# Performance work log

Hardware: AMD Instinct MI355X
Metric: run time of the kernel (lower is better)

The kernel has to match this reference:

```python
import jax, jax.numpy as jnp
import numpy as np

EPS = 1e-8
NUM_LAYERS = 6


def setup_inputs() -> dict:
    key = jax.random.key(0)
    ks = jax.random.split(key, 8)
    N, Cin, Cout, S, H, W = 4, 256, 256, 512, 64, 64
    fan_in = Cin  # kaiming for 1x1 conv, leaky_relu a=0 -> gain sqrt(2)
    return {
        "x": jax.random.normal(ks[0], (N, Cin, H, W), dtype=jnp.float32),
        "y": jax.random.normal(ks[1], (N, S), dtype=jnp.float32),
        "ch_conv_w": jax.random.normal(ks[2], (Cout, Cin), dtype=jnp.float32) / np.sqrt(fan_in),
        "ch_conv_b": jnp.zeros((Cout,), dtype=jnp.float32),
        "affine_w": jax.random.normal(ks[3], (NUM_LAYERS, Cout, S), dtype=jnp.float32) / np.sqrt(S),
        "affine_b": jnp.zeros((NUM_LAYERS, Cout), dtype=jnp.float32),
        "mod_w": jax.random.normal(ks[4], (NUM_LAYERS, Cout, Cout), dtype=jnp.float32) * np.sqrt(2.0 / Cout),
    }


def _forward(x, y, ch_conv_w, ch_conv_b, affine_w, affine_b, mod_w):
    # 1x1 channel conv (with bias)
    x = jnp.einsum("oi,bihw->bohw", ch_conv_w, x) + ch_conv_b[None, :, None, None]
    x = jnp.repeat(jnp.repeat(x, 2, axis=2), 2, axis=3)
    # channel repeat_interleave(2) -> [N, 2C, H, W]
    x = jnp.repeat(x, 2, axis=1)

    C = x.shape[1] // 2
    for i in range(NUM_LAYERS):
        x1, x2 = x[:, :C], x[:, C:]
        # SpatialShift2d with default directions pads [1,1,1,1] (replicate) then
        # crops the identical region for every split -> exact identity.
        y1 = x1 + x2
        # g-branch: Conv2dMod(k=1) with per-sample style modulation + exact GELU
        s = jnp.einsum("cs,bs->bc", affine_w[i], y) + affine_b[i]  # [B, C]
        wmod = mod_w[i][None] * (s[:, :, None] + 1.0)              # [B, O, I] (style scales OUTPUT channel)
        d = jax.lax.rsqrt(jnp.sum(wmod * wmod, axis=2, keepdims=True) + EPS)
        wmod = wmod * d
        h = jnp.einsum("boi,bihw->bohw", wmod, y1)
        y2 = x2 + jax.nn.gelu(h, approximate=False)
        x = jnp.concatenate([y1, y2], axis=1)

    x1, x2 = x[:, :C], x[:, C:]
    return (x1 + x2) * 0.5


def reference(x, y, ch_conv_w, ch_conv_b, affine_w, affine_b, mod_w):
    return _forward(x, y, ch_conv_w, ch_conv_b, affine_w, affine_b, mod_w)
```

## Files before the change

### kernel.cpp

```cpp
#include <hip/hip_runtime.h>
#include <math.h>

#define NB 4
#define CC 256
#define SS 512
#define NL 6
#define SLOT_HW 65536

typedef __attribute__((ext_vector_type(8))) short s16x8;
typedef __attribute__((ext_vector_type(4))) float f32x4;
typedef __attribute__((ext_vector_type(4))) unsigned short u16x4;
typedef __attribute__((ext_vector_type(8))) unsigned short u16x8;

__device__ __forceinline__ unsigned short f2bf(float f) {
    unsigned u = __builtin_bit_cast(unsigned, f);
    u += 0x7FFFu + ((u >> 16) & 1u);
    return (unsigned short)(u >> 16);
}
__device__ __forceinline__ float bf2f(unsigned short h) {
    unsigned u = ((unsigned)h) << 16;
    return __builtin_bit_cast(float, u);
}
__device__ __forceinline__ float gelu_fast(float x) {
    float u = x * (1.0f + 0.044715f * x * x);
    float e = __expf(-1.5957691216f * u);
    return x / (1.0f + e);
}


__global__ __launch_bounds__(256) void wmod_kernel(
    const float* __restrict__ y, const float* __restrict__ aw,
    const float* __restrict__ ab, const float* __restrict__ mw,
    unsigned short* __restrict__ wsBF)
{
    int w = threadIdx.x >> 6, lane = threadIdx.x & 63;
    int r = blockIdx.x*4 + w;
    int l = r >> 10;
    int b = (r >> 8) & 3;
    int o = r & 255;

    const float* awr = aw + (size_t)(l*CC + o)*SS;
    const float* yb  = y + (size_t)b*SS;
    float s = 0.f;
#pragma unroll
    for (int j = 0; j < 8; ++j) { int idx = lane + 64*j; s += awr[idx]*yb[idx]; }
#pragma unroll
    for (int off = 32; off; off >>= 1) s += __shfl_xor(s, off);
    float t = s + ab[l*CC + o] + 1.0f;

    const float* mwr = mw + (size_t)(l*CC + o)*CC;
    float wv[4]; float ss = 0.f;
#pragma unroll
    for (int u = 0; u < 4; ++u) { int j = lane + 64*u; wv[u] = mwr[j]*t; ss += wv[u]*wv[u]; }
#pragma unroll
    for (int off = 32; off; off >>= 1) ss += __shfl_xor(ss, off);
    float d = 1.0f / sqrtf(ss + 1e-8f);

    unsigned short* slot = wsBF + (size_t)(1 + l*NB + b)*SLOT_HW;
#pragma unroll
    for (int u = 0; u < 4; ++u) {
        int k = lane + 64*u;
        int f = (o >> 4)*8 + (k >> 5);
        int hw = f*512 + ((k >> 3) & 3)*128 + (o & 15)*8 + (k & 7);
        slot[hw] = f2bf(wv[u]*d);
    }
}

__global__ __launch_bounds__(256) void cwsplit_kernel(
    const float* __restrict__ cw, unsigned short* __restrict__ wsBF)
{
    int w = threadIdx.x >> 6, lane = threadIdx.x & 63;
    int m = blockIdx.x*4 + w;
#pragma unroll
    for (int u = 0; u < 4; ++u) {
        int k = lane + 64*u;
        int f = (m >> 4)*8 + (k >> 5);
        int hw = f*512 + ((k >> 3) & 3)*128 + (m & 15)*8 + (k & 7);
        wsBF[hw] = f2bf(cw[(size_t)m*CC + k]);
    }
}

#define BFRAG(buf, nt, kcl, hl) \
    (lds + (buf)*16384 + ((((nt)*2 + (kcl))*2 + (hl)))*1024)

__global__ __launch_bounds__(512, 2) void fused_kernel(
    const float* __restrict__ x, const float* __restrict__ cb,
    const unsigned short* __restrict__ wsBF, float* __restrict__ out)
{
    __shared__ __align__(16) unsigned char lds[50176];
    float* xS = (float*)(lds + 32768);
    float* S2 = (float*)lds;

    const int tid  = threadIdx.x;
    const int lane = tid & 63;
    const int wid  = tid >> 6;
    const int wm   = wid >> 1;
    const int wn   = wid & 1;
    const int l15  = lane & 15;
    const int q    = lane >> 4;

    const int bswz  = blockIdx.x & 7;
    const int b     = bswz >> 1;
    const int strip = ((blockIdx.x >> 3) << 1) | (bswz & 1);
    const int n0    = strip * 64;

    float y1[4][2][4], y2[4][2][4];
    f32x4 acc[4][2];

#pragma unroll
    for (int t = 0; t < 4; ++t)
#pragma unroll
        for (int s = 0; s < 2; ++s) acc[t][s] = 0;

    for (int kq = 0; kq < 4; ++kq) {
        int buf = kq & 1;
        {
            int r0 = tid >> 4, c4 = (tid & 15) * 4;
#pragma unroll
            for (int p = 0; p < 2; ++p) {
                int row = r0 + 32*p;
                float4 v = *(const float4*)&x[((size_t)(b*CC + kq*64 + row))*4096 + n0 + c4];
                *(float4*)&xS[row*68 + c4] = v;
            }
        }
        __syncthreads();
        {
            int n = tid & 63, k0 = (tid >> 6) * 8;
            float f[8];
#pragma unroll
            for (int i = 0; i < 8; ++i) f[i] = xS[(k0+i)*68 + n];
            u16x8 hv, lv;
#pragma unroll
            for (int i = 0; i < 8; ++i) {
                unsigned short h = f2bf(f[i]);
                hv[i] = h; lv[i] = f2bf(f[i] - bf2f(h));
            }
            int nt = n >> 4, n15 = n & 15, kcl = k0 >> 5, qq = (k0 >> 3) & 3;
            *(u16x8*)(BFRAG(buf,nt,kcl,0) + (16*qq + n15)*16) = hv;
            *(u16x8*)(BFRAG(buf,nt,kcl,1) + (16*qq + n15)*16) = lv;
        }
        s16x8 afr[2][4];
#pragma unroll
        for (int kcl = 0; kcl < 2; ++kcl)
#pragma unroll
        for (int t = 0; t < 4; ++t)
            afr[kcl][t] = *(const s16x8*)(wsBF + (size_t)((4*wm+t)*8 + kq*2+kcl)*512 + lane*8);
        __syncthreads();
#pragma unroll
        for (int kcl = 0; kcl < 2; ++kcl)
#pragma unroll
        for (int s = 0; s < 2; ++s) {
            int nt = 2*wn + s;
            s16x8 bh = *(const s16x8*)(BFRAG(buf,nt,kcl,0) + lane*16);
            s16x8 bl = *(const s16x8*)(BFRAG(buf,nt,kcl,1) + lane*16);
#pragma unroll
            for (int t = 0; t < 4; ++t) {
                acc[t][s] = __builtin_amdgcn_mfma_f32_16x16x32_bf16(afr[kcl][t], bh, acc[t][s], 0, 0, 0);
                acc[t][s] = __builtin_amdgcn_mfma_f32_16x16x32_bf16(afr[kcl][t], bl, acc[t][s], 0, 0, 0);
            }
        }
    }

#pragma unroll
    for (int pass = 0; pass < 2; ++pass) {
        __syncthreads();
        if ((wm >> 1) == pass) {
#pragma unroll
            for (int t = 0; t < 4; ++t)
#pragma unroll
            for (int s = 0; s < 2; ++s)
#pragma unroll
            for (int r = 0; r < 4; ++r) {
                int m  = 64*wm + 16*t + 4*q + r;
                int nl = 32*wn + 16*s + l15;
                S2[(m - 128*pass)*66 + nl] = acc[t][s][r] + cb[m];
            }
        }
        __syncthreads();
#pragma unroll
        for (int t = 0; t < 4; ++t)
#pragma unroll
        for (int s = 0; s < 2; ++s)
#pragma unroll
        for (int r = 0; r < 4; ++r) {
            int c  = 64*wm + 16*t + 4*q + r;
            int nl = 32*wn + 16*s + l15;
            float v = S2[(c >> 1)*66 + nl];
            if (pass == 0) { y1[t][s][r] = v; }
            else           { y2[t][s][r] = v; y1[t][s][r] += v; }
        }
    }
    __syncthreads();

    for (int l = 0; l < NL; ++l) {
        const unsigned short* slot = wsBF + (size_t)(1 + l*NB + b)*SLOT_HW;
#pragma unroll
        for (int t = 0; t < 4; ++t)
#pragma unroll
            for (int s = 0; s < 2; ++s) acc[t][s] = 0;

        for (int kq = 0; kq < 4; ++kq) {
            int buf = kq & 1;
            if (wm == kq) {
#pragma unroll
                for (int t = 0; t < 4; ++t)
#pragma unroll
                for (int s = 0; s < 2; ++s) {
                    int nt = 2*wn + s, kcl = t >> 1;
                    int qq = 2*(t & 1) + (q >> 1), jb = 4*(q & 1);
                    u16x4 hv, lv;
#pragma unroll
                    for (int r = 0; r < 4; ++r) {
                        unsigned short h = f2bf(y1[t][s][r]);
                        hv[r] = h; lv[r] = f2bf(y1[t][s][r] - bf2f(h));
                    }
                    *(u16x4*)(BFRAG(buf,nt,kcl,0) + (16*qq + l15)*16 + jb*2) = hv;
                    *(u16x4*)(BFRAG(buf,nt,kcl,1) + (16*qq + l15)*16 + jb*2) = lv;
                }
            }
            s16x8 afr[2][4];
#pragma unroll
            for (int kcl = 0; kcl < 2; ++kcl)
#pragma unroll
            for (int t = 0; t < 4; ++t)
                afr[kcl][t] = *(const s16x8*)(slot + (size_t)((4*wm+t)*8 + kq*2+kcl)*512 + lane*8);
            __syncthreads();
#pragma unroll
            for (int kcl = 0; kcl < 2; ++kcl)
#pragma unroll
            for (int s = 0; s < 2; ++s) {
                int nt = 2*wn + s;
                s16x8 bh = *(const s16x8*)(BFRAG(buf,nt,kcl,0) + lane*16);
                s16x8 bl = *(const s16x8*)(BFRAG(buf,nt,kcl,1) + lane*16);
#pragma unroll
                for (int t = 0; t < 4; ++t) {
                    acc[t][s] = __builtin_amdgcn_mfma_f32_16x16x32_bf16(afr[kcl][t], bh, acc[t][s], 0, 0, 0);
                    acc[t][s] = __builtin_amdgcn_mfma_f32_16x16x32_bf16(afr[kcl][t], bl, acc[t][s], 0, 0, 0);
                }
            }
        }
#pragma unroll
        for (int t = 0; t < 4; ++t)
#pragma unroll
        for (int s = 0; s < 2; ++s)
#pragma unroll
        for (int r = 0; r < 4; ++r) {
            y2[t][s][r] += gelu_fast(acc[t][s][r]);
            if (l < NL - 1) y1[t][s][r] += y2[t][s][r];
        }
    }

#pragma unroll
    for (int t = 0; t < 4; ++t)
#pragma unroll
    for (int s = 0; s < 2; ++s)
#pragma unroll
    for (int r = 0; r < 4; ++r) {
        int ch = 64*wm + 16*t + 4*q + r;
        int w  = 32*wn + 16*s + l15;
        float v = 0.5f*(y1[t][s][r] + y2[t][s][r]);
        float2 vv = make_float2(v, v);
        size_t base = (((size_t)(b*CC + ch)*128 + 2*strip))*128 + 2*w;
        *(float2*)&out[base]       = vv;
        *(float2*)&out[base + 128] = vv;
    }
}

extern "C" void kernel_launch(void* const* d_in, const int* in_sizes, int n_in,
                              void* d_out, int out_size, void* d_ws, size_t ws_size,
                              hipStream_t stream) {
    const float* x  = (const float*)d_in[0];
    const float* y  = (const float*)d_in[1];
    const float* cw = (const float*)d_in[2];
    const float* cb = (const float*)d_in[3];
    const float* aw = (const float*)d_in[4];
    const float* ab = (const float*)d_in[5];
    const float* mw = (const float*)d_in[6];
    float* out = (float*)d_out;

    unsigned short* wsBF = (unsigned short*)d_ws;

    wmod_kernel<<<NL*NB*CC/4, 256, 0, stream>>>(y, aw, ab, mw, wsBF);
    cwsplit_kernel<<<64, 256, 0, stream>>>(cw, wsBF);
    fused_kernel<<<256, 512, 0, stream>>>(x, cb, wsBF, out);
}
```

Baseline: 141.1 us.

## Stage full K panel in LDS per layer, cut barriers, prefetch A fragments

```diff
diff --git a/kernel.cpp b/kernel.cpp
--- a/kernel.cpp
+++ b/kernel.cpp
@@ -9,6 +9,7 @@
 
 typedef __attribute__((ext_vector_type(8))) short s16x8;
 typedef __attribute__((ext_vector_type(4))) float f32x4;
+typedef __attribute__((ext_vector_type(2))) float f32x2;
 typedef __attribute__((ext_vector_type(4))) unsigned short u16x4;
 typedef __attribute__((ext_vector_type(8))) unsigned short u16x8;
 
@@ -80,15 +81,15 @@
     }
 }
 
-#define BFRAG(buf, nt, kcl, hl) \
-    (lds + (buf)*16384 + ((((nt)*2 + (kcl))*2 + (hl)))*1024)
+#define BFRAG(nt, kq, kcl, hl) \
+    (lds + (((((nt)*4 + (kq))*2 + (kcl))*2 + (hl)))*1024)
 
 __global__ __launch_bounds__(512, 2) void fused_kernel(
     const float* __restrict__ x, const float* __restrict__ cb,
     const unsigned short* __restrict__ wsBF, float* __restrict__ out)
 {
-    __shared__ __align__(16) unsigned char lds[50176];
-    float* xS = (float*)(lds + 32768);
+    __shared__ __align__(16) unsigned char lds[82944];
+    float* xS = (float*)(lds + 65536);
     float* S2 = (float*)lds;
 
     const int tid  = threadIdx.x;
@@ -113,7 +114,6 @@
         for (int s = 0; s < 2; ++s) acc[t][s] = 0;
 
     for (int kq = 0; kq < 4; ++kq) {
-        int buf = kq & 1;
         {
             int r0 = tid >> 4, c4 = (tid & 15) * 4;
 #pragma unroll
@@ -136,8 +136,8 @@
                 hv[i] = h; lv[i] = f2bf(f[i] - bf2f(h));
             }
             int nt = n >> 4, n15 = n & 15, kcl = k0 >> 5, qq = (k0 >> 3) & 3;
-            *(u16x8*)(BFRAG(buf,nt,kcl,0) + (16*qq + n15)*16) = hv;
-            *(u16x8*)(BFRAG(buf,nt,kcl,1) + (16*qq + n15)*16) = lv;
+            *(u16x8*)(BFRAG(nt,kq,kcl,0) + (16*qq + n15)*16) = hv;
+            *(u16x8*)(BFRAG(nt,kq,kcl,1) + (16*qq + n15)*16) = lv;
         }
         s16x8 afr[2][4];
 #pragma unroll
@@ -151,8 +151,8 @@
 #pragma unroll
         for (int s = 0; s < 2; ++s) {
             int nt = 2*wn + s;
-            s16x8 bh = *(const s16x8*)(BFRAG(buf,nt,kcl,0) + lane*16);
-            s16x8 bl = *(const s16x8*)(BFRAG(buf,nt,kcl,1) + lane*16);
+            s16x8 bh = *(const s16x8*)(BFRAG(nt,kq,kcl,0) + lane*16);
+            s16x8 bl = *(const s16x8*)(BFRAG(nt,kq,kcl,1) + lane*16);
 #pragma unroll
             for (int t = 0; t < 4; ++t) {
                 acc[t][s] = __builtin_amdgcn_mfma_f32_16x16x32_bf16(afr[kcl][t], bh, acc[t][s], 0, 0, 0);
@@ -199,43 +199,45 @@
 #pragma unroll
             for (int s = 0; s < 2; ++s) acc[t][s] = 0;
 
-        for (int kq = 0; kq < 4; ++kq) {
-            int buf = kq & 1;
-            if (wm == kq) {
+#pragma unroll
+        for (int t = 0; t < 4; ++t)
+#pragma unroll
+        for (int s = 0; s < 2; ++s) {
+            int nt = 2*wn + s, kcl = t >> 1;
+            int qq = 2*(t & 1) + (q >> 1), jb = 4*(q & 1);
+            u16x4 hv, lv;
+#pragma unroll
+            for (int r = 0; r < 4; ++r) {
+                unsigned short h = f2bf(y1[t][s][r]);
+                hv[r] = h; lv[r] = f2bf(y1[t][s][r] - bf2f(h));
+            }
+            *(u16x4*)(BFRAG(nt,wm,kcl,0) + (16*qq + l15)*16 + jb*2) = hv;
+            *(u16x4*)(BFRAG(nt,wm,kcl,1) + (16*qq + l15)*16 + jb*2) = lv;
+        }
+        s16x8 aN[4], aC[4];
+#pragma unroll
+        for (int t = 0; t < 4; ++t)
+            aN[t] = *(const s16x8*)(slot + (size_t)((4*wm+t)*8 + 0)*512 + lane*8);
+        __syncthreads();
+#pragma unroll
+        for (int step = 0; step < 8; ++step) {
+#pragma unroll
+            for (int t = 0; t < 4; ++t) aC[t] = aN[t];
+            if (step < 7) {
 #pragma unroll
                 for (int t = 0; t < 4; ++t)
-#pragma unroll
-                for (int s = 0; s < 2; ++s) {
-                    int nt = 2*wn + s, kcl = t >> 1;
-                    int qq = 2*(t & 1) + (q >> 1), jb = 4*(q & 1);
-                    u16x4 hv, lv;
-#pragma unroll
-                    for (int r = 0; r < 4; ++r) {
-                        unsigned short h = f2bf(y1[t][s][r]);
-                        hv[r] = h; lv[r] = f2bf(y1[t][s][r] - bf2f(h));
-                    }
-                    *(u16x4*)(BFRAG(buf,nt,kcl,0) + (16*qq + l15)*16 + jb*2) = hv;
-                    *(u16x4*)(BFRAG(buf,nt,kcl,1) + (16*qq + l15)*16 + jb*2) = lv;
-                }
-            }
-            s16x8 afr[2][4];
-#pragma unroll
-            for (int kcl = 0; kcl < 2; ++kcl)
-#pragma unroll
-            for (int t = 0; t < 4; ++t)
-                afr[kcl][t] = *(const s16x8*)(slot + (size_t)((4*wm+t)*8 + kq*2+kcl)*512 + lane*8);
-            __syncthreads();
-#pragma unroll
-            for (int kcl = 0; kcl < 2; ++kcl)
+                    aN[t] = *(const s16x8*)(slot + (size_t)((4*wm+t)*8 + step+1)*512 + lane*8);
+            }
+            int kq = step >> 1, kcl = step & 1;
 #pragma unroll
             for (int s = 0; s < 2; ++s) {
                 int nt = 2*wn + s;
-                s16x8 bh = *(const s16x8*)(BFRAG(buf,nt,kcl,0) + lane*16);
-                s16x8 bl = *(const s16x8*)(BFRAG(buf,nt,kcl,1) + lane*16);
+                s16x8 bh = *(const s16x8*)(BFRAG(nt,kq,kcl,0) + lane*16);
+                s16x8 bl = *(const s16x8*)(BFRAG(nt,kq,kcl,1) + lane*16);
 #pragma unroll
                 for (int t = 0; t < 4; ++t) {
-                    acc[t][s] = __builtin_amdgcn_mfma_f32_16x16x32_bf16(afr[kcl][t], bh, acc[t][s], 0, 0, 0);
-                    acc[t][s] = __builtin_amdgcn_mfma_f32_16x16x32_bf16(afr[kcl][t], bl, acc[t][s], 0, 0, 0);
+                    acc[t][s] = __builtin_amdgcn_mfma_f32_16x16x32_bf16(aC[t], bh, acc[t][s], 0, 0, 0);
+                    acc[t][s] = __builtin_amdgcn_mfma_f32_16x16x32_bf16(aC[t], bl, acc[t][s], 0, 0, 0);
                 }
             }
         }
@@ -248,6 +250,7 @@
             y2[t][s][r] += gelu_fast(acc[t][s][r]);
             if (l < NL - 1) y1[t][s][r] += y2[t][s][r];
         }
+        __syncthreads();
     }
 
 #pragma unroll
@@ -259,10 +262,10 @@
         int ch = 64*wm + 16*t + 4*q + r;
         int w  = 32*wn + 16*s + l15;
         float v = 0.5f*(y1[t][s][r] + y2[t][s][r]);
-        float2 vv = make_float2(v, v);
+        f32x2 vv = {v, v};
         size_t base = (((size_t)(b*CC + ch)*128 + 2*strip))*128 + 2*w;
-        *(float2*)&out[base]       = vv;
-        *(float2*)&out[base + 128] = vv;
+        __builtin_nontemporal_store(vv, (f32x2*)&out[base]);
+        __builtin_nontemporal_store(vv, (f32x2*)&out[base + 128]);
     }
 }
 
```

Measured after the change: 140.5 us. Within noise of the previous version (-0.4%).
